# Optimization experiments

Hardware: AMD Instinct MI355X
Metric: run time of the kernel (lower is better)

## Reference

```python
import jax, jax.numpy as jnp
import numpy as np

NEG_SLOPE = 0.2  # PyG GATConv LeakyReLU slope
EPS = 1e-16


def _add_self_loops(edge_index, num_nodes):
    loops = jnp.arange(num_nodes, dtype=edge_index.dtype)
    return jnp.concatenate([edge_index, jnp.stack([loops, loops])], axis=1)


def _gat_conv(x, src, dst, W, a_src, a_dst, bias, heads, out_ch, concat, num_nodes):
    # x: [N, F_in]; W: [F_in, heads*out_ch]
    h = (x @ W).reshape(num_nodes, heads, out_ch)            # [N, H, C]
    alpha_s = jnp.einsum('nhc,hc->nh', h, a_src)              # [N, H]
    alpha_d = jnp.einsum('nhc,hc->nh', h, a_dst)              # [N, H]
    e = jax.nn.leaky_relu(alpha_s[src] + alpha_d[dst], NEG_SLOPE)  # [E, H]
    # segment softmax over incoming edges of each destination node
    e_max = jax.ops.segment_max(e, dst, num_segments=num_nodes)
    e = jnp.exp(e - e_max[dst])
    denom = jax.ops.segment_sum(e, dst, num_segments=num_nodes)
    alpha = e / (denom[dst] + EPS)                             # [E, H]
    msg = h[src] * alpha[:, :, None]                           # [E, H, C]
    out = jax.ops.segment_sum(msg, dst, num_segments=num_nodes)  # [N, H, C]
    out = out.reshape(num_nodes, heads * out_ch) if concat else out.mean(axis=1)
    return out + bias


def setup_inputs() -> dict:
    key = jax.random.key(0)
    ks = jax.random.split(key, 10)
    N, F_in, H, C1, classes, E = 50000, 128, 8, 16, 40, 1600000
    return {
        'x': jax.random.normal(ks[0], (N, F_in), jnp.float32),
        'edge_index': jax.random.randint(ks[1], (2, E), 0, N, jnp.int64),
        'W1': jax.random.normal(ks[2], (F_in, H * C1), jnp.float32) * (1.0 / np.sqrt(F_in)),
        'a_src1': jax.random.normal(ks[3], (H, C1), jnp.float32) * 0.1,
        'a_dst1': jax.random.normal(ks[4], (H, C1), jnp.float32) * 0.1,
        'b1': jax.random.normal(ks[5], (H * C1,), jnp.float32) * 0.01,
        'W2': jax.random.normal(ks[6], (H * C1, classes), jnp.float32) * (1.0 / np.sqrt(H * C1)),
        'a_src2': jax.random.normal(ks[7], (1, classes), jnp.float32) * 0.1,
        'a_dst2': jax.random.normal(ks[8], (1, classes), jnp.float32) * 0.1,
        'b2': jax.random.normal(ks[9], (classes,), jnp.float32) * 0.01,
    }


def reference(x, edge_index, W1, a_src1, a_dst1, b1, W2, a_src2, a_dst2, b2):
    N = x.shape[0]
    ei = _add_self_loops(edge_index, N)
    src, dst = ei[0], ei[1]
    h = _gat_conv(x, src, dst, W1, a_src1, a_dst1, b1, heads=8, out_ch=16, concat=True, num_nodes=N)
    h = jax.nn.elu(h)
    out = _gat_conv(h, src, dst, W2, a_src2, a_dst2, b2, heads=1, out_ch=40, concat=False, num_nodes=N)
    return out
```

## Files before the change

### kernel.cpp

```cpp
#include <hip/hip_runtime.h>
#include <hip/hip_bf16.h>
#include <hip/hip_fp16.h>

#define NEG_SLOPE 0.2f
#define EPSV 1e-16f
#define CAP 96
#define CHUNK 4096
#define BCAP 9216

static __device__ __forceinline__ float lrelu(float v) {
    return v > 0.0f ? v : NEG_SLOPE * v;
}
static __device__ __forceinline__ float eluf(float v) {
    return v > 0.0f ? v : (__expf(v) - 1.0f);
}

__global__ __launch_bounds__(256) void k_fused1(
    const float* __restrict__ x, const float* __restrict__ W,
    const float* __restrict__ a_src, const float* __restrict__ a_dst,
    const int* __restrict__ ei, int E, int N, int AB,
    __half* __restrict__ h, float* __restrict__ as, float* __restrict__ ad,
    int* __restrict__ gcur, unsigned* __restrict__ bbuf) {
    __shared__ float wl[64 * 128];
    __shared__ float xl[32 * 64];
    const int tid = threadIdx.x;

    if ((int)blockIdx.x < AB) {
        int* cnt = (int*)wl;
        int* base = ((int*)wl) + 256;
        int e0 = blockIdx.x * CHUNK;
        int e1 = e0 + CHUNK < E ? e0 + CHUNK : E;
        cnt[tid] = 0;
        __syncthreads();
        for (int e = e0 + tid; e < e1; e += 256)
            atomicAdd(&cnt[ei[E + e] >> 8], 1);
        __syncthreads();
        {
            int c = cnt[tid];
            base[tid] = c ? atomicAdd(&gcur[tid], c) : 0;
            cnt[tid] = 0;
        }
        __syncthreads();
        for (int e = e0 + tid; e < e1; e += 256) {
            int s = ei[e];
            int d = ei[E + e];
            int b = d >> 8;
            int k = atomicAdd(&cnt[b], 1);
            bbuf[(size_t)b * BCAP + base[b] + k] =
                (unsigned)s | ((unsigned)(d & 255) << 16);
        }
        return;
    }

    const int row0 = (blockIdx.x - AB) * 32;
    const int c0 = (tid & 31) * 4;
    const int r0 = (tid >> 5) * 4;
    float acc[4][4];
#pragma unroll
    for (int r = 0; r < 4; ++r)
#pragma unroll
        for (int c = 0; c < 4; ++c) acc[r][c] = 0.0f;

    for (int kt = 0; kt < 128; kt += 64) {
        __syncthreads();
#pragma unroll
        for (int i = tid * 4; i < 64 * 128; i += 1024)
            *(float4*)&wl[i] = *(const float4*)&W[kt * 128 + i];
#pragma unroll
        for (int i = tid * 4; i < 32 * 64; i += 1024) {
            int r = i >> 6, c = i & 63;
            int gr = row0 + r;
            float4 v = make_float4(0.f, 0.f, 0.f, 0.f);
            if (gr < N) v = *(const float4*)&x[(size_t)gr * 128 + kt + c];
            *(float4*)&xl[i] = v;
        }
        __syncthreads();
#pragma unroll 8
        for (int k = 0; k < 64; ++k) {
            float4 w4 = *(const float4*)&wl[k * 128 + c0];
#pragma unroll
            for (int r = 0; r < 4; ++r) {
                float xv = xl[(r0 + r) * 64 + k];
                acc[r][0] = fmaf(xv, w4.x, acc[r][0]);
                acc[r][1] = fmaf(xv, w4.y, acc[r][1]);
                acc[r][2] = fmaf(xv, w4.z, acc[r][2]);
                acc[r][3] = fmaf(xv, w4.w, acc[r][3]);
            }
        }
    }
#pragma unroll
    for (int r = 0; r < 4; ++r) {
        int gr = row0 + r0 + r;
        if (gr < N) {
            __half2 q0 = __floats2half2_rn(acc[r][0], acc[r][1]);
            __half2 q1 = __floats2half2_rn(acc[r][2], acc[r][3]);
            uint2 st;
            st.x = *(unsigned*)&q0;
            st.y = *(unsigned*)&q1;
            *(uint2*)&h[(size_t)gr * 128 + c0] = st;
        }
    }
    float4 asv = *(const float4*)&a_src[c0];
    float4 adv = *(const float4*)&a_dst[c0];
#pragma unroll
    for (int r = 0; r < 4; ++r) {
        float sp = acc[r][0] * asv.x + acc[r][1] * asv.y + acc[r][2] * asv.z +
                   acc[r][3] * asv.w;
        float dp = acc[r][0] * adv.x + acc[r][1] * adv.y + acc[r][2] * adv.z +
                   acc[r][3] * adv.w;
        sp += __shfl_xor(sp, 1, 64);
        sp += __shfl_xor(sp, 2, 64);
        dp += __shfl_xor(dp, 1, 64);
        dp += __shfl_xor(dp, 2, 64);
        int gr = row0 + r0 + r;
        if ((tid & 3) == 0 && gr < N) {
            int hd = (tid & 31) >> 2;
            as[(size_t)gr * 8 + hd] = sp;
            ad[(size_t)gr * 8 + hd] = dp;
        }
    }
}

__global__ __launch_bounds__(256) void k_csr2(const unsigned* __restrict__ bbuf,
                                              const int* __restrict__ gcnt, int N,
                                              int* __restrict__ deg,
                                              unsigned short* __restrict__ srcs) {
    __shared__ unsigned short rows[256 * CAP];
    __shared__ int cnt[256];
    const int b = blockIdx.x, tid = threadIdx.x;
    cnt[tid] = 0;
    __syncthreads();
    int nb = gcnt[b];
    const unsigned* bp = &bbuf[(size_t)b * BCAP];
    for (int i = tid; i < nb; i += 256) {
        unsigned u = bp[i];
        int dlo = u >> 16;
        int k = atomicAdd(&cnt[dlo], 1);
        rows[dlo * CAP + k] = (unsigned short)(u & 0xFFFFu);
    }
    __syncthreads();
    int n = (b << 8) + tid;
    if (n < N) deg[n] = cnt[tid];
    int maxn = N - (b << 8);
    if (maxn > 256) maxn = 256;
    if (maxn < 0) maxn = 0;
    const unsigned* r32 = (const unsigned*)rows;
    unsigned* g32 = (unsigned*)srcs;
    size_t gbase = (size_t)(b << 8) * (CAP / 2);
    int lim = maxn * (CAP / 2);
    for (int i = tid; i < lim; i += 256) g32[gbase + i] = r32[i];
}

__global__ __launch_bounds__(256) void k_agg1(const int* __restrict__ deg,
                                              const unsigned short* __restrict__ srcs,
                                              const float* __restrict__ as1,
                                              const float* __restrict__ ad1,
                                              const __half* __restrict__ h1,
                                              const float* __restrict__ b1,
                                              float* __restrict__ hout, int N) {
    int wid = threadIdx.x >> 6, lane = threadIdx.x & 63;
    int n = blockIdx.x * 4 + wid;
    if (n >= N) return;
    size_t st = (size_t)n * CAP;
    int tot = deg[n] + 1;
    int half = lane >> 5;
    int cl = lane & 31;
    int h = cl >> 2;
    int c0 = cl * 4;
    float myad = ad1[(size_t)n * 8 + h];
    float l = 0.f;
    float4 acc = make_float4(0.f, 0.f, 0.f, 0.f);

    for (int base = 0; base < tot; base += 64) {
        int rem = tot - base;
        if (rem > 64) rem = 64;
        int gi = base + lane;
        int sreg = (gi < tot - 1) ? (int)srcs[st + gi] : n;
        for (int t = 0; t < rem; t += 4) {
            int myi0 = t + half;
            int myi1 = t + 2 + half;
            int s0 = __shfl(sreg, myi0, 64);
            int s1 = __shfl(sreg, myi1, 64);
            float av0 = as1[(size_t)s0 * 8 + h];
            float av1 = as1[(size_t)s1 * 8 + h];
            uint2 u0 = *(const uint2*)&h1[(size_t)s0 * 128 + c0];
            uint2 u1 = *(const uint2*)&h1[(size_t)s1 * 128 + c0];
            float p0 = __expf(lrelu(av0 + myad));
            float p1 = __expf(lrelu(av1 + myad));
            if (myi0 >= rem) p0 = 0.f;
            if (myi1 >= rem) p1 = 0.f;
            l += p0 + p1;
            float2 f00 = __half22float2(*(const __half2*)&u0.x);
            float2 f01 = __half22float2(*(const __half2*)&u0.y);
            float2 f10 = __half22float2(*(const __half2*)&u1.x);
            float2 f11 = __half22float2(*(const __half2*)&u1.y);
            acc.x = fmaf(p0, f00.x, acc.x);
            acc.y = fmaf(p0, f00.y, acc.y);
            acc.z = fmaf(p0, f01.x, acc.z);
            acc.w = fmaf(p0, f01.y, acc.w);
            acc.x = fmaf(p1, f10.x, acc.x);
            acc.y = fmaf(p1, f10.y, acc.y);
            acc.z = fmaf(p1, f11.x, acc.z);
            acc.w = fmaf(p1, f11.y, acc.w);
        }
    }
    l += __shfl_xor(l, 32, 64);
    acc.x += __shfl_xor(acc.x, 32, 64);
    acc.y += __shfl_xor(acc.y, 32, 64);
    acc.z += __shfl_xor(acc.z, 32, 64);
    acc.w += __shfl_xor(acc.w, 32, 64);
    if (half == 0) {
        float rl = 1.f / (l + EPSV);
        float4 bb = *(const float4*)&b1[c0];
        acc.x = eluf(fmaf(acc.x, rl, bb.x));
        acc.y = eluf(fmaf(acc.y, rl, bb.y));
        acc.z = eluf(fmaf(acc.z, rl, bb.z));
        acc.w = eluf(fmaf(acc.w, rl, bb.w));
        *(float4*)&hout[(size_t)n * 128 + c0] = acc;
    }
}

__global__ __launch_bounds__(256) void k_gemm2(const float* __restrict__ hin,
                                               const float* __restrict__ W2,
                                               const float* __restrict__ a2s,
                                               const float* __restrict__ a2d,
                                               __half* __restrict__ h2,
                                               float* __restrict__ as2,
                                               float* __restrict__ ad2, int N) {
    __shared__ float wl[128 * 40];
    __shared__ float xl[4 * 128];
    const int tid = threadIdx.x;
    const int n0 = blockIdx.x * 4;
#pragma unroll
    for (int i = tid * 4; i < 128 * 40; i += 1024)
        *(float4*)&wl[i] = *(const float4*)&W2[i];
    {
        int i = tid * 2;
        int r = i >> 7;
        int gr = n0 + r;
        float2 v = make_float2(0.f, 0.f);
        if (gr < N) v = *(const float2*)&hin[(size_t)gr * 128 + (i & 127)];
        *(float2*)&xl[i] = v;
    }
    __syncthreads();
    const int r = tid >> 6, c = tid & 63;
    const int gr = n0 + r;
    float acc = 0.f;
    if (c < 40) {
        const float* xr = &xl[r * 128];
#pragma unroll 8
        for (int k = 0; k < 128; ++k) acc = fmaf(xr[k], wl[k * 40 + c], acc);
    }
    float sv = (c < 40) ? acc * a2s[c] : 0.f;
    float dv = (c < 40) ? acc * a2d[c] : 0.f;
#pragma unroll
    for (int o = 32; o > 0; o >>= 1) {
        sv += __shfl_down(sv, o, 64);
        dv += __shfl_down(dv, o, 64);
    }
    if (gr < N) {
        if (c < 40) h2[(size_t)gr * 40 + c] = __float2half(acc);
        if (c == 0) {
            as2[gr] = sv;
            ad2[gr] = dv;
        }
    }
}

__global__ __launch_bounds__(256) void k_agg2(const int* __restrict__ deg,
                                              const unsigned short* __restrict__ srcs,
                                              const float* __restrict__ as2,
                                              const float* __restrict__ ad2,
                                              const __half* __restrict__ h2,
                                              const float* __restrict__ b2,
                                              float* __restrict__ out, int N) {
    int wid = threadIdx.x >> 6, lane = threadIdx.x & 63;
    int n = blockIdx.x * 4 + wid;
    if (n >= N) return;
    size_t st = (size_t)n * CAP;
    int tot = deg[n] + 1;
    int half = lane >> 5;
    int cl = lane & 31;
    int c0 = cl * 2;
    float adv = ad2[n];
    float l = 0.f;
    float2 acc = make_float2(0.f, 0.f);

    for (int base = 0; base < tot; base += 64) {
        int rem = tot - base;
        if (rem > 64) rem = 64;
        int gi = base + lane;
        int sreg = (gi < tot - 1) ? (int)srcs[st + gi] : n;
        for (int t = 0; t < rem; t += 4) {
            int myi0 = t + half;
            int myi1 = t + 2 + half;
            int s0 = __shfl(sreg, myi0, 64);
            int s1 = __shfl(sreg, myi1, 64);
            float p0 = __expf(lrelu(as2[s0] + adv));
            float p1 = __expf(lrelu(as2[s1] + adv));
            if (myi0 >= rem) p0 = 0.f;
            if (myi1 >= rem) p1 = 0.f;
            l += p0 + p1;
            if (cl < 20) {
                float2 hv0 = __half22float2(*(const __half2*)&h2[(size_t)s0 * 40 + c0]);
                float2 hv1 = __half22float2(*(const __half2*)&h2[(size_t)s1 * 40 + c0]);
                acc.x = fmaf(p0, hv0.x, acc.x);
                acc.y = fmaf(p0, hv0.y, acc.y);
                acc.x = fmaf(p1, hv1.x, acc.x);
                acc.y = fmaf(p1, hv1.y, acc.y);
            }
        }
    }
    l += __shfl_xor(l, 32, 64);
    acc.x += __shfl_xor(acc.x, 32, 64);
    acc.y += __shfl_xor(acc.y, 32, 64);
    if (half == 0 && cl < 20) {
        float rl = 1.f / (l + EPSV);
        out[(size_t)n * 40 + c0]     = fmaf(acc.x, rl, b2[c0]);
        out[(size_t)n * 40 + c0 + 1] = fmaf(acc.y, rl, b2[c0 + 1]);
    }
}

extern "C" void kernel_launch(void* const* d_in, const int* in_sizes, int n_in,
                              void* d_out, int out_size, void* d_ws, size_t ws_size,
                              hipStream_t stream) {
    const float* x      = (const float*)d_in[0];
    const int*   ei     = (const int*)d_in[1];
    const float* W1     = (const float*)d_in[2];
    const float* a_src1 = (const float*)d_in[3];
    const float* a_dst1 = (const float*)d_in[4];
    const float* b1     = (const float*)d_in[5];
    const float* W2     = (const float*)d_in[6];
    const float* a_src2 = (const float*)d_in[7];
    const float* a_dst2 = (const float*)d_in[8];
    const float* b2     = (const float*)d_in[9];
    float* out = (float*)d_out;

    const int N = in_sizes[0] / 128;
    const int E = in_sizes[1] / 2;
    const int AB = (E + CHUNK - 1) / CHUNK;
    const int GB = (N + 31) / 32;
    const int NBUCK = (N + 255) >> 8;

    float* ws = (float*)d_ws;
    size_t off = 0;
    auto alloc = [&](size_t nElem) {
        float* p = ws + off;
        off += (nElem + 3) & ~(size_t)3;
        return p;
    };
    __half* h1           = (__half*)alloc((size_t)N * 64);
    float* hin2          = alloc((size_t)N * 128);
    float* as1           = alloc((size_t)N * 8);
    float* ad1           = alloc((size_t)N * 8);
    __half* h2           = (__half*)alloc((size_t)N * 20);
    float* as2           = alloc(N);
    float* ad2           = alloc(N);
    int* deg             = (int*)alloc(N);
    int* gcur            = (int*)alloc(256);
    unsigned short* srcs = (unsigned short*)alloc(((size_t)N * CAP + 1) / 2);
    unsigned* bbuf       = (unsigned*)hin2;

    hipMemsetAsync(deg, 0, ((size_t)N + 256) * sizeof(int), stream);

    dim3 B(256);
    k_fused1<<<dim3(AB + GB), B, 0, stream>>>(x, W1, a_src1, a_dst1, ei, E, N, AB,
                                              h1, as1, ad1, gcur, bbuf);
    k_csr2<<<dim3(NBUCK), B, 0, stream>>>(bbuf, gcur, N, deg, srcs);
    k_agg1<<<dim3((N + 3) / 4), B, 0, stream>>>(deg, srcs, as1, ad1, h1, b1, hin2, N);
    k_gemm2<<<dim3((N + 3) / 4), B, 0, stream>>>(hin2, W2, a_src2, a_dst2, h2, as2, ad2, N);
    k_agg2<<<dim3((N + 3) / 4), B, 0, stream>>>(deg, srcs, as2, ad2, h2, b2, out, N);
}
```

Before: 225.7 us.

## Restructure agg1/agg2 edge loops, batch bucket loads, and double rows per gemm2 block

k_fused1's bucketing pass now loads its 16 destination indices into registers once and reuses them for both the counting and scatter passes. k_agg1 is remapped so each lane handles 8 channels through 16-byte loads, and one exp per (edge, head) is computed and broadcast by shuffle rather than recomputed per channel lane. k_agg2 computes each edge's attention weight once per lane and shuffles it, and k_gemm2 processes 8 rows per block so each W2 shared-memory read feeds two accumulators. The aim is fewer redundant exp and gather loads and fewer global re-reads, at the cost of more registers and shuffles.

```diff
diff --git a/kernel.cpp b/kernel.cpp
--- a/kernel.cpp
+++ b/kernel.cpp
@@ -29,11 +29,17 @@
         int* cnt = (int*)wl;
         int* base = ((int*)wl) + 256;
         int e0 = blockIdx.x * CHUNK;
-        int e1 = e0 + CHUNK < E ? e0 + CHUNK : E;
+        int dreg[16];
+#pragma unroll
+        for (int jj = 0; jj < 16; ++jj) {
+            int e = e0 + tid + jj * 256;
+            dreg[jj] = (e < E) ? ei[E + e] : -1;
+        }
         cnt[tid] = 0;
         __syncthreads();
-        for (int e = e0 + tid; e < e1; e += 256)
-            atomicAdd(&cnt[ei[E + e] >> 8], 1);
+#pragma unroll
+        for (int jj = 0; jj < 16; ++jj)
+            if (dreg[jj] >= 0) atomicAdd(&cnt[dreg[jj] >> 8], 1);
         __syncthreads();
         {
             int c = cnt[tid];
@@ -41,13 +47,17 @@
             cnt[tid] = 0;
         }
         __syncthreads();
-        for (int e = e0 + tid; e < e1; e += 256) {
-            int s = ei[e];
-            int d = ei[E + e];
-            int b = d >> 8;
-            int k = atomicAdd(&cnt[b], 1);
-            bbuf[(size_t)b * BCAP + base[b] + k] =
-                (unsigned)s | ((unsigned)(d & 255) << 16);
+#pragma unroll
+        for (int jj = 0; jj < 16; ++jj) {
+            int e = e0 + tid + jj * 256;
+            if (e < E) {
+                int s = ei[e];
+                int d = dreg[jj];
+                int b = d >> 8;
+                int k = atomicAdd(&cnt[b], 1);
+                bbuf[(size_t)b * BCAP + base[b] + k] =
+                    (unsigned)s | ((unsigned)(d & 255) << 16);
+            }
         }
         return;
     }
@@ -163,60 +173,66 @@
     if (n >= N) return;
     size_t st = (size_t)n * CAP;
     int tot = deg[n] + 1;
-    int half = lane >> 5;
-    int cl = lane & 31;
-    int h = cl >> 2;
-    int c0 = cl * 4;
-    float myad = ad1[(size_t)n * 8 + h];
+    int q = lane >> 4;
+    int j = lane & 15;
+    int es = lane >> 3;
+    int hq = lane & 7;
+    float adv = ad1[(size_t)n * 8 + hq];
     float l = 0.f;
-    float4 acc = make_float4(0.f, 0.f, 0.f, 0.f);
+    float acc[8];
+#pragma unroll
+    for (int k = 0; k < 8; ++k) acc[k] = 0.f;
 
     for (int base = 0; base < tot; base += 64) {
         int rem = tot - base;
         if (rem > 64) rem = 64;
         int gi = base + lane;
         int sreg = (gi < tot - 1) ? (int)srcs[st + gi] : n;
-        for (int t = 0; t < rem; t += 4) {
-            int myi0 = t + half;
-            int myi1 = t + 2 + half;
-            int s0 = __shfl(sreg, myi0, 64);
-            int s1 = __shfl(sreg, myi1, 64);
-            float av0 = as1[(size_t)s0 * 8 + h];
-            float av1 = as1[(size_t)s1 * 8 + h];
-            uint2 u0 = *(const uint2*)&h1[(size_t)s0 * 128 + c0];
-            uint2 u1 = *(const uint2*)&h1[(size_t)s1 * 128 + c0];
-            float p0 = __expf(lrelu(av0 + myad));
-            float p1 = __expf(lrelu(av1 + myad));
-            if (myi0 >= rem) p0 = 0.f;
-            if (myi1 >= rem) p1 = 0.f;
-            l += p0 + p1;
-            float2 f00 = __half22float2(*(const __half2*)&u0.x);
-            float2 f01 = __half22float2(*(const __half2*)&u0.y);
-            float2 f10 = __half22float2(*(const __half2*)&u1.x);
-            float2 f11 = __half22float2(*(const __half2*)&u1.y);
-            acc.x = fmaf(p0, f00.x, acc.x);
-            acc.y = fmaf(p0, f00.y, acc.y);
-            acc.z = fmaf(p0, f01.x, acc.z);
-            acc.w = fmaf(p0, f01.y, acc.w);
-            acc.x = fmaf(p1, f10.x, acc.x);
-            acc.y = fmaf(p1, f10.y, acc.y);
-            acc.z = fmaf(p1, f11.x, acc.z);
-            acc.w = fmaf(p1, f11.y, acc.w);
-        }
-    }
+        for (int bb = 0; bb < rem; bb += 8) {
+            int sp = __shfl(sreg, bb + es, 64);
+            float pv = __expf(lrelu(as1[(size_t)sp * 8 + hq] + adv));
+            if (bb + es >= rem) pv = 0.f;
+            l += pv;
+#pragma unroll
+            for (int t = 0; t < 8; t += 4) {
+                int er = t + q;
+                int s = __shfl(sreg, bb + er, 64);
+                float p = __shfl(pv, (er << 3) | (j >> 1), 64);
+                uint4 u = *(const uint4*)&h1[(size_t)s * 128 + (j << 3)];
+                const __half2* hp2 = (const __half2*)&u;
+#pragma unroll
+                for (int k2 = 0; k2 < 4; ++k2) {
+                    float2 f = __half22float2(hp2[k2]);
+                    acc[2 * k2]     = fmaf(p, f.x, acc[2 * k2]);
+                    acc[2 * k2 + 1] = fmaf(p, f.y, acc[2 * k2 + 1]);
+                }
+            }
+        }
+    }
+#pragma unroll
+    for (int k = 0; k < 8; ++k) {
+        acc[k] += __shfl_xor(acc[k], 16, 64);
+        acc[k] += __shfl_xor(acc[k], 32, 64);
+    }
+    l += __shfl_xor(l, 8, 64);
+    l += __shfl_xor(l, 16, 64);
     l += __shfl_xor(l, 32, 64);
-    acc.x += __shfl_xor(acc.x, 32, 64);
-    acc.y += __shfl_xor(acc.y, 32, 64);
-    acc.z += __shfl_xor(acc.z, 32, 64);
-    acc.w += __shfl_xor(acc.w, 32, 64);
-    if (half == 0) {
-        float rl = 1.f / (l + EPSV);
-        float4 bb = *(const float4*)&b1[c0];
-        acc.x = eluf(fmaf(acc.x, rl, bb.x));
-        acc.y = eluf(fmaf(acc.y, rl, bb.y));
-        acc.z = eluf(fmaf(acc.z, rl, bb.z));
-        acc.w = eluf(fmaf(acc.w, rl, bb.w));
-        *(float4*)&hout[(size_t)n * 128 + c0] = acc;
+    float myl = __shfl(l, j >> 1, 64);
+    if (q == 0) {
+        float rl = 1.f / (myl + EPSV);
+        float4 bb0 = *(const float4*)&b1[j * 8];
+        float4 bb1 = *(const float4*)&b1[j * 8 + 4];
+        float4 o0, o1;
+        o0.x = eluf(fmaf(acc[0], rl, bb0.x));
+        o0.y = eluf(fmaf(acc[1], rl, bb0.y));
+        o0.z = eluf(fmaf(acc[2], rl, bb0.z));
+        o0.w = eluf(fmaf(acc[3], rl, bb0.w));
+        o1.x = eluf(fmaf(acc[4], rl, bb1.x));
+        o1.y = eluf(fmaf(acc[5], rl, bb1.y));
+        o1.z = eluf(fmaf(acc[6], rl, bb1.z));
+        o1.w = eluf(fmaf(acc[7], rl, bb1.w));
+        *(float4*)&hout[(size_t)n * 128 + j * 8] = o0;
+        *(float4*)&hout[(size_t)n * 128 + j * 8 + 4] = o1;
     }
 }
 
@@ -228,42 +244,52 @@
                                                float* __restrict__ as2,
                                                float* __restrict__ ad2, int N) {
     __shared__ float wl[128 * 40];
-    __shared__ float xl[4 * 128];
+    __shared__ float xl[8 * 128];
     const int tid = threadIdx.x;
-    const int n0 = blockIdx.x * 4;
+    const int n0 = blockIdx.x * 8;
 #pragma unroll
     for (int i = tid * 4; i < 128 * 40; i += 1024)
         *(float4*)&wl[i] = *(const float4*)&W2[i];
     {
-        int i = tid * 2;
+        int i = tid * 4;
         int r = i >> 7;
         int gr = n0 + r;
-        float2 v = make_float2(0.f, 0.f);
-        if (gr < N) v = *(const float2*)&hin[(size_t)gr * 128 + (i & 127)];
-        *(float2*)&xl[i] = v;
+        float4 v = make_float4(0.f, 0.f, 0.f, 0.f);
+        if (gr < N) v = *(const float4*)&hin[(size_t)gr * 128 + (i & 127)];
+        *(float4*)&xl[i] = v;
     }
     __syncthreads();
-    const int r = tid >> 6, c = tid & 63;
-    const int gr = n0 + r;
-    float acc = 0.f;
+    const int w = tid >> 6, c = tid & 63;
+    float accA = 0.f, accB = 0.f;
     if (c < 40) {
-        const float* xr = &xl[r * 128];
+        const float* xa = &xl[(2 * w) * 128];
+        const float* xb = &xl[(2 * w + 1) * 128];
 #pragma unroll 8
-        for (int k = 0; k < 128; ++k) acc = fmaf(xr[k], wl[k * 40 + c], acc);
-    }
-    float sv = (c < 40) ? acc * a2s[c] : 0.f;
-    float dv = (c < 40) ? acc * a2d[c] : 0.f;
+        for (int k = 0; k < 128; ++k) {
+            float wv = wl[k * 40 + c];
+            accA = fmaf(xa[k], wv, accA);
+            accB = fmaf(xb[k], wv, accB);
+        }
+    }
+    float svA = (c < 40) ? accA * a2s[c] : 0.f;
+    float dvA = (c < 40) ? accA * a2d[c] : 0.f;
+    float svB = (c < 40) ? accB * a2s[c] : 0.f;
+    float dvB = (c < 40) ? accB * a2d[c] : 0.f;
 #pragma unroll
     for (int o = 32; o > 0; o >>= 1) {
-        sv += __shfl_down(sv, o, 64);
-        dv += __shfl_down(dv, o, 64);
-    }
-    if (gr < N) {
-        if (c < 40) h2[(size_t)gr * 40 + c] = __float2half(acc);
-        if (c == 0) {
-            as2[gr] = sv;
-            ad2[gr] = dv;
-        }
+        svA += __shfl_down(svA, o, 64);
+        dvA += __shfl_down(dvA, o, 64);
+        svB += __shfl_down(svB, o, 64);
+        dvB += __shfl_down(dvB, o, 64);
+    }
+    int grA = n0 + 2 * w, grB = grA + 1;
+    if (grA < N) {
+        if (c < 40) h2[(size_t)grA * 40 + c] = __float2half(accA);
+        if (c == 0) { as2[grA] = svA; ad2[grA] = dvA; }
+    }
+    if (grB < N) {
+        if (c < 40) h2[(size_t)grB * 40 + c] = __float2half(accB);
+        if (c == 0) { as2[grB] = svB; ad2[grB] = dvB; }
     }
 }
 
@@ -291,27 +317,22 @@
         if (rem > 64) rem = 64;
         int gi = base + lane;
         int sreg = (gi < tot - 1) ? (int)srcs[st + gi] : n;
-        for (int t = 0; t < rem; t += 4) {
-            int myi0 = t + half;
-            int myi1 = t + 2 + half;
-            int s0 = __shfl(sreg, myi0, 64);
-            int s1 = __shfl(sreg, myi1, 64);
-            float p0 = __expf(lrelu(as2[s0] + adv));
-            float p1 = __expf(lrelu(as2[s1] + adv));
-            if (myi0 >= rem) p0 = 0.f;
-            if (myi1 >= rem) p1 = 0.f;
-            l += p0 + p1;
+        float pv = 0.f;
+        if (gi < tot) pv = __expf(lrelu(as2[sreg] + adv));
+        l += pv;
+        for (int t = 0; t < rem; t += 2) {
+            int myi = t + half;
+            int s = __shfl(sreg, myi, 64);
+            float p = __shfl(pv, myi, 64);
             if (cl < 20) {
-                float2 hv0 = __half22float2(*(const __half2*)&h2[(size_t)s0 * 40 + c0]);
-                float2 hv1 = __half22float2(*(const __half2*)&h2[(size_t)s1 * 40 + c0]);
-                acc.x = fmaf(p0, hv0.x, acc.x);
-                acc.y = fmaf(p0, hv0.y, acc.y);
-                acc.x = fmaf(p1, hv1.x, acc.x);
-                acc.y = fmaf(p1, hv1.y, acc.y);
+                float2 hv = __half22float2(*(const __half2*)&h2[(size_t)s * 40 + c0]);
+                acc.x = fmaf(p, hv.x, acc.x);
+                acc.y = fmaf(p, hv.y, acc.y);
             }
         }
     }
-    l += __shfl_xor(l, 32, 64);
+#pragma unroll
+    for (int off = 1; off < 64; off <<= 1) l += __shfl_xor(l, off, 64);
     acc.x += __shfl_xor(acc.x, 32, 64);
     acc.y += __shfl_xor(acc.y, 32, 64);
     if (half == 0 && cl < 20) {
@@ -368,6 +389,6 @@
                                               h1, as1, ad1, gcur, bbuf);
     k_csr2<<<dim3(NBUCK), B, 0, stream>>>(bbuf, gcur, N, deg, srcs);
     k_agg1<<<dim3((N + 3) / 4), B, 0, stream>>>(deg, srcs, as1, ad1, h1, b1, hin2, N);
-    k_gemm2<<<dim3((N + 3) / 4), B, 0, stream>>>(hin2, W2, a_src2, a_dst2, h2, as2, ad2, N);
+    k_gemm2<<<dim3((N + 7) / 8), B, 0, stream>>>(hin2, W2, a_src2, a_dst2, h2, as2, ad2, N);
     k_agg2<<<dim3((N + 3) / 4), B, 0, stream>>>(deg, srcs, as2, ad2, h2, b2, out, N);
 }
```

Result: faster. 211.4 us (-6.3%).
